# Performance work log

Hardware: AMD Instinct MI355X
Metric: run time of the kernel (lower is better)

The kernel has to match this reference:

```python
import jax, jax.numpy as jnp
import numpy as np

N, E = 50000, 800000
IN_FEATS, EDGE_FEATS = 256, 64
H, F = 8, 32  # num_heads, out_feats
LRELU_SLOPE = 0.01  # nn.LeakyReLU() default (module ignores alpha arg)


def setup_inputs() -> dict:
    key = jax.random.key(0)
    ks = jax.random.split(key, 9)
    return {
        "h": jax.random.normal(ks[0], (N, IN_FEATS), jnp.float32),
        "edge_features": jax.random.normal(ks[1], (E, EDGE_FEATS), jnp.float32),
        "src": jax.random.randint(ks[2], (E,), 0, N, jnp.int32),
        "dst": jax.random.randint(ks[3], (E,), 0, N, jnp.int32),
        "W_w": jax.random.normal(ks[4], (IN_FEATS, H * F), jnp.float32) * 0.05,
        "We_w": jax.random.normal(ks[5], (EDGE_FEATS, H * F), jnp.float32) * 0.05,
        "a_src": jax.random.normal(ks[6], (H, F), jnp.float32) * 0.1,
        "a_dst": jax.random.normal(ks[7], (H, F), jnp.float32) * 0.1,
        "a_edge": jax.random.normal(ks[8], (H, F), jnp.float32) * 0.1,
    }


def reference(h, edge_features, src, dst, W_w, We_w, a_src, a_dst, a_edge):
    # Node / edge linear projections -> [N,H,F], [E,H,F]
    Wh = (h @ W_w).reshape(-1, H, F)
    We = (edge_features @ We_w).reshape(-1, H, F)

    # Per-edge attention logits [E,H]: score = src.a_src + dst.a_dst + e.a_edge
    s = (jnp.einsum('ehf,hf->eh', Wh[src], a_src)
         + jnp.einsum('ehf,hf->eh', Wh[dst], a_dst)
         + jnp.einsum('ehf,hf->eh', We, a_edge))
    s = jnp.where(s > 0, s, LRELU_SLOPE * s)

    # Segment softmax over incoming edges of each dst node
    m = jax.ops.segment_max(s, dst, num_segments=N)          # [N,H]
    ex = jnp.exp(s - m[dst])                                 # [E,H]
    den = jax.ops.segment_sum(ex, dst, num_segments=N)       # [N,H]
    a = ex / den[dst]                                        # [E,H]

    # Weighted scatter-sum aggregation (dropout is identity at p=0 / eval)
    msg = Wh[src] * a[:, :, None]                            # [E,H,F]
    h_new = jax.ops.segment_sum(msg, dst, num_segments=N)    # [N,H,F]

    # concat=True path: reshape + ELU
    h_new = h_new.reshape(-1, H * F)
    return jax.nn.elu(h_new)
```

## Files before the change

### kernel.cpp

```cpp
#include <hip/hip_runtime.h>

#define N_NODES 50000
#define N_EDGES 800000
#define HEADS 8
#define FOUT 32
#define HF 256
#define IN_F 256
#define EDGE_F 64
#define SCAN_BLOCKS 196
#define HIST_BLOCKS 3125
#define CVTW_BLOCKS 256

typedef __attribute__((ext_vector_type(8))) short bf16x8;
typedef __attribute__((ext_vector_type(4))) float f32x4;

__device__ inline ushort f2bf(float f) {
  unsigned u = __float_as_uint(f);
  unsigned r = 0x7FFFu + ((u >> 16) & 1u);
  return (ushort)((u + r) >> 16);
}

__global__ __launch_bounds__(256) void k_misc(
    const int* __restrict__ dst, int* __restrict__ deg,
    const float* __restrict__ W, ushort* __restrict__ Wt,
    const float* __restrict__ We_w, const float* __restrict__ a_edge,
    float* __restrict__ Bmat)
{
  int b = blockIdx.x;
  if (b < HIST_BLOCKS) {
    int e = b * 256 + threadIdx.x;
    atomicAdd(&deg[dst[e]], 1);
  } else if (b < HIST_BLOCKS + CVTW_BLOCKS) {
    int i = (b - HIST_BLOCKS) * 256 + threadIdx.x;
    int n = i >> 8, k = i & 255;
    Wt[i] = f2bf(W[k * HF + n]);
  } else {
    int i = (b - HIST_BLOCKS - CVTW_BLOCKS) * 256 + threadIdx.x;
    if (i < EDGE_F * HEADS) {
      int k = i >> 3, h = i & 7;
      float s = 0.f;
#pragma unroll
      for (int f = 0; f < FOUT; ++f)
        s += We_w[k * HF + h * FOUT + f] * a_edge[h * FOUT + f];
      Bmat[i] = s;
    }
  }
}

__global__ __launch_bounds__(256) void k_gemm_fused(
    const float* __restrict__ A,
    const ushort* __restrict__ Wt,
    const float* __restrict__ a_src, const float* __restrict__ a_dst,
    ushort* __restrict__ Whb,
    float* __restrict__ alpha_s, float* __restrict__ alpha_d, int M)
{
  __shared__ ushort As[64 * 40];
  __shared__ ushort Bs[256 * 40];
  const int tid = threadIdx.x;
  const int wave = tid >> 6, lane = tid & 63;
  const int m0 = blockIdx.x * 64;
  const int row16 = lane & 15;
  const int kg = lane >> 4;
  f32x4 acc[4][4] = {};

  const int a_r = tid >> 2;
  const int a_c = (tid & 3) * 8;
  const int a_row = m0 + a_r;

  for (int k0 = 0; k0 < IN_F; k0 += 32) {
    uint4 av = make_uint4(0, 0, 0, 0);
    if (a_row < M) {
      float4 f0 = *(const float4*)&A[(size_t)a_row * IN_F + k0 + a_c];
      float4 f1 = *(const float4*)&A[(size_t)a_row * IN_F + k0 + a_c + 4];
      av.x = (unsigned)f2bf(f0.x) | ((unsigned)f2bf(f0.y) << 16);
      av.y = (unsigned)f2bf(f0.z) | ((unsigned)f2bf(f0.w) << 16);
      av.z = (unsigned)f2bf(f1.x) | ((unsigned)f2bf(f1.y) << 16);
      av.w = (unsigned)f2bf(f1.z) | ((unsigned)f2bf(f1.w) << 16);
    }
    *(uint4*)&As[a_r * 40 + a_c] = av;
    const uint4* bp = (const uint4*)&Wt[(size_t)tid * IN_F + k0];
    uint4 b0 = bp[0], b1 = bp[1];
    *(uint4*)&Bs[tid * 40 + 0] = b0;
    *(uint4*)&Bs[tid * 40 + 8] = b1;
    uint4 b2 = bp[2], b3 = bp[3];
    *(uint4*)&Bs[tid * 40 + 16] = b2;
    *(uint4*)&Bs[tid * 40 + 24] = b3;
    __syncthreads();
    bf16x8 af[4], bfr[4];
#pragma unroll
    for (int mi = 0; mi < 4; ++mi)
      af[mi] = *(const bf16x8*)&As[(mi * 16 + row16) * 40 + kg * 8];
#pragma unroll
    for (int ni = 0; ni < 4; ++ni)
      bfr[ni] = *(const bf16x8*)&Bs[(wave * 64 + ni * 16 + row16) * 40 + kg * 8];
#pragma unroll
    for (int mi = 0; mi < 4; ++mi)
#pragma unroll
      for (int ni = 0; ni < 4; ++ni)
        acc[mi][ni] = __builtin_amdgcn_mfma_f32_16x16x32_bf16(af[mi], bfr[ni], acc[mi][ni], 0, 0, 0);
    __syncthreads();
  }

  float cs[4], cd[4];
#pragma unroll
  for (int ni = 0; ni < 4; ++ni) {
    int hh = 2 * wave + (ni >> 1);
    int ff = (ni & 1) * 16 + row16;
    cs[ni] = a_src[hh * FOUT + ff];
    cd[ni] = a_dst[hh * FOUT + ff];
  }
#pragma unroll
  for (int mi = 0; mi < 4; ++mi) {
#pragma unroll
    for (int r = 0; r < 4; ++r) {
      int row = m0 + mi * 16 + kg * 4 + r;
      float ps0 = acc[mi][0][r] * cs[0] + acc[mi][1][r] * cs[1];
      float ps1 = acc[mi][2][r] * cs[2] + acc[mi][3][r] * cs[3];
      float pd0 = acc[mi][0][r] * cd[0] + acc[mi][1][r] * cd[1];
      float pd1 = acc[mi][2][r] * cd[2] + acc[mi][3][r] * cd[3];
#pragma unroll
      for (int msk = 1; msk <= 8; msk <<= 1) {
        ps0 += __shfl_xor(ps0, msk, 64);
        ps1 += __shfl_xor(ps1, msk, 64);
        pd0 += __shfl_xor(pd0, msk, 64);
        pd1 += __shfl_xor(pd1, msk, 64);
      }
      if (row16 == 0 && row < M) {
        *(float2*)&alpha_s[row * 8 + 2 * wave] = make_float2(ps0, ps1);
        *(float2*)&alpha_d[row * 8 + 2 * wave] = make_float2(pd0, pd1);
      }
      if (row < M) {
#pragma unroll
        for (int ni = 0; ni < 4; ++ni)
          Whb[(size_t)row * HF + wave * 64 + ni * 16 + row16] = f2bf(acc[mi][ni][r]);
      }
    }
  }
}

__global__ __launch_bounds__(256) void k_scanA(const int* __restrict__ deg,
                                               int* __restrict__ blockSums)
{
  __shared__ int ws[4];
  int idx = blockIdx.x * 256 + threadIdx.x;
  int v = (idx < N_NODES) ? deg[idx] : 0;
  int s = v;
#pragma unroll
  for (int off = 32; off > 0; off >>= 1)
    s += __shfl_xor(s, off, 64);
  if ((threadIdx.x & 63) == 0) ws[threadIdx.x >> 6] = s;
  __syncthreads();
  if (threadIdx.x == 0)
    blockSums[blockIdx.x] = ws[0] + ws[1] + ws[2] + ws[3];
}

__global__ __launch_bounds__(256) void k_scanC(const int* __restrict__ deg,
                                               const int* __restrict__ blockSums,
                                               int* __restrict__ offsets,
                                               int* __restrict__ cursor)
{
  __shared__ int tmp[256];
  __shared__ int s_base;
  int t = threadIdx.x;
  int v = (t < SCAN_BLOCKS) ? blockSums[t] : 0;
  tmp[t] = v;
  __syncthreads();
  int x = v;
  for (int off = 1; off < 256; off <<= 1) {
    int y = (t >= off) ? tmp[t - off] : 0;
    __syncthreads();
    x += y;
    tmp[t] = x;
    __syncthreads();
  }
  if (t == (int)blockIdx.x) s_base = x - v;
  if (blockIdx.x == 0 && t == 255) offsets[N_NODES] = x;
  __syncthreads();
  int base = s_base;
  int idx = blockIdx.x * 256 + t;
  int d = (idx < N_NODES) ? deg[idx] : 0;
  tmp[t] = d;
  __syncthreads();
  int x2 = d;
  for (int off = 1; off < 256; off <<= 1) {
    int y = (t >= off) ? tmp[t - off] : 0;
    __syncthreads();
    x2 += y;
    tmp[t] = x2;
    __syncthreads();
  }
  if (idx < N_NODES) {
    int pre = base + x2 - d;
    offsets[idx] = pre;
    cursor[idx] = pre;
  }
}

__global__ __launch_bounds__(256) void k_sedge(
    const float* __restrict__ ef, const int* __restrict__ src,
    const int* __restrict__ dst, const float* __restrict__ alpha_s,
    const float* __restrict__ alpha_d, const float* __restrict__ Bmat,
    int* __restrict__ cursor, float* __restrict__ s8,
    int2* __restrict__ srcE)
{
  __shared__ float Bs[EDGE_F * HEADS];
  for (int i = threadIdx.x; i < EDGE_F * HEADS; i += 256) Bs[i] = Bmat[i];
  __syncthreads();
  const int t = threadIdx.x;
  const int q = t & 3;
  const int e = blockIdx.x * 64 + (t >> 2);
  const int sn = src[e], dn = dst[e];

  float sc[8] = {};
  const float4* efr = (const float4*)&ef[(size_t)e * EDGE_F + q * 16];
#pragma unroll
  for (int g = 0; g < 4; ++g) {
    float4 v = efr[g];
    const float* b0 = &Bs[(q * 16 + g * 4) * 8];
#pragma unroll
    for (int hh = 0; hh < 8; ++hh)
      sc[hh] += v.x * b0[hh] + v.y * b0[8 + hh] + v.z * b0[16 + hh] + v.w * b0[24 + hh];
  }
#pragma unroll
  for (int hh = 0; hh < 8; ++hh) {
    sc[hh] += __shfl_xor(sc[hh], 1, 64);
    sc[hh] += __shfl_xor(sc[hh], 2, 64);
  }
  float2 as = *(const float2*)&alpha_s[sn * 8 + 2 * q];
  float2 ad = *(const float2*)&alpha_d[dn * 8 + 2 * q];
  float a0 = sc[2 * q] + as.x + ad.x;
  float a1 = sc[2 * q + 1] + as.y + ad.y;
  a0 = a0 > 0.f ? a0 : 0.01f * a0;
  a1 = a1 > 0.f ? a1 : 0.01f * a1;
  *(float2*)&s8[(size_t)e * 8 + 2 * q] = make_float2(a0, a1);
  if (q == 0) {
    int p = atomicAdd(&cursor[dn], 1);
    srcE[p] = make_int2(sn, e);
  }
}

__global__ __launch_bounds__(256) void k_agg(
    const float* __restrict__ s8, const int2* __restrict__ srcE,
    const int* __restrict__ offsets, const uint* __restrict__ Whb_u,
    float* __restrict__ out)
{
  const int n = blockIdx.x * 4 + (threadIdx.x >> 6);
  const int l = threadIdx.x & 63;
  const int beg = offsets[n], end = offsets[n + 1];
  const int h_sm = l & 7;
  const int es = l >> 3;
  const int h0 = l >> 4;
  const int h1 = 4 + h0;

  float m_run = -3.0e38f, l_run = 0.f;
  float acc00 = 0.f, acc01 = 0.f, acc10 = 0.f, acc11 = 0.f;

  int rx = 0;
  float s_cur = -3.0e38f;
  if (beg + es < end) {
    int2 r = srcE[beg + es];
    rx = r.x;
    s_cur = s8[(size_t)r.y * 8 + h_sm];
  }

  for (int c0 = beg; c0 < end; c0 += 8) {
    const int cnt = min(8, end - c0);
    int rx_n = 0;
    float s_n = -3.0e38f;
    if (c0 + 8 + es < end) {
      int2 r = srcE[c0 + 8 + es];
      rx_n = r.x;
      s_n = s8[(size_t)r.y * 8 + h_sm];
    }
    float s = s_cur;
    float mc = s;
    mc = fmaxf(mc, __shfl_xor(mc, 8, 64));
    mc = fmaxf(mc, __shfl_xor(mc, 16, 64));
    mc = fmaxf(mc, __shfl_xor(mc, 32, 64));
    float m_new = fmaxf(m_run, mc);
    float f = __expf(m_run - m_new);
    float w = __expf(s - m_new);
    float ws = w;
    ws += __shfl_xor(ws, 8, 64);
    ws += __shfl_xor(ws, 16, 64);
    ws += __shfl_xor(ws, 32, 64);
    l_run = l_run * f + ws;
    m_run = m_new;
    float f0 = __shfl(f, h0, 64);
    float f1 = __shfl(f, h1, 64);
    acc00 *= f0; acc01 *= f0; acc10 *= f1; acc11 *= f1;
    if (cnt == 8) {
#pragma unroll
      for (int k = 0; k < 8; ++k) {
        int idx = __shfl(rx, k << 3, 64);
        float w0 = __shfl(w, (k << 3) | h0, 64);
        float w1 = __shfl(w, (k << 3) | h1, 64);
        const uint* rowp = Whb_u + ((size_t)idx << 7);
        uint v0 = rowp[l];
        uint v1 = rowp[l + 64];
        acc00 = fmaf(w0, __uint_as_float(v0 << 16), acc00);
        acc01 = fmaf(w0, __uint_as_float(v0 & 0xFFFF0000u), acc01);
        acc10 = fmaf(w1, __uint_as_float(v1 << 16), acc10);
        acc11 = fmaf(w1, __uint_as_float(v1 & 0xFFFF0000u), acc11);
      }
    } else {
      for (int k = 0; k < cnt; ++k) {
        int idx = __shfl(rx, k << 3, 64);
        float w0 = __shfl(w, (k << 3) | h0, 64);
        float w1 = __shfl(w, (k << 3) | h1, 64);
        const uint* rowp = Whb_u + ((size_t)idx << 7);
        uint v0 = rowp[l];
        uint v1 = rowp[l + 64];
        acc00 = fmaf(w0, __uint_as_float(v0 << 16), acc00);
        acc01 = fmaf(w0, __uint_as_float(v0 & 0xFFFF0000u), acc01);
        acc10 = fmaf(w1, __uint_as_float(v1 << 16), acc10);
        acc11 = fmaf(w1, __uint_as_float(v1 & 0xFFFF0000u), acc11);
      }
    }
    rx = rx_n;
    s_cur = s_n;
  }

  float l0 = __shfl(l_run, h0, 64);
  float l1 = __shfl(l_run, h1, 64);
  float inv0 = (l0 > 0.f) ? 1.f / l0 : 0.f;
  float inv1 = (l1 > 0.f) ? 1.f / l1 : 0.f;
  acc00 *= inv0; acc01 *= inv0; acc10 *= inv1; acc11 *= inv1;

  float2 oA, oB;
  oA.x = acc00 > 0.f ? acc00 : expm1f(acc00);
  oA.y = acc01 > 0.f ? acc01 : expm1f(acc01);
  oB.x = acc10 > 0.f ? acc10 : expm1f(acc10);
  oB.y = acc11 > 0.f ? acc11 : expm1f(acc11);
  *(float2*)&out[(size_t)n * HF + 2 * l] = oA;
  *(float2*)&out[(size_t)n * HF + 128 + 2 * l] = oB;
}

extern "C" void kernel_launch(void* const* d_in, const int* in_sizes, int n_in,
                              void* d_out, int out_size, void* d_ws, size_t ws_size,
                              hipStream_t stream)
{
  const float* h    = (const float*)d_in[0];
  const float* ef   = (const float*)d_in[1];
  const int*   src  = (const int*)d_in[2];
  const int*   dst  = (const int*)d_in[3];
  const float* W_w  = (const float*)d_in[4];
  const float* We_w = (const float*)d_in[5];
  const float* a_s  = (const float*)d_in[6];
  const float* a_d  = (const float*)d_in[7];
  const float* a_e  = (const float*)d_in[8];
  float* out = (float*)d_out;

  char* ws = (char*)d_ws;
  size_t off = 0;
  auto take = [&](size_t bytes) {
    char* p = ws + off;
    off += (bytes + 255) & ~(size_t)255;
    return p;
  };
  ushort* Whb     = (ushort*)take((size_t)N_NODES * HF * 2);
  float* s8       = (float*)take((size_t)N_EDGES * HEADS * 4);
  float* alpha_s  = (float*)take((size_t)N_NODES * HEADS * 4);
  float* alpha_d  = (float*)take((size_t)N_NODES * HEADS * 4);
  int2*  srcE     = (int2*)take((size_t)N_EDGES * 8);
  int*   deg      = (int*)take((size_t)N_NODES * 4);
  int*   offs     = (int*)take((size_t)(N_NODES + 1) * 4);
  int*   cursor   = (int*)take((size_t)N_NODES * 4);
  float* Bmat     = (float*)take((size_t)EDGE_F * HEADS * 4);
  ushort* Wt      = (ushort*)take((size_t)HF * IN_F * 2);
  int*   blockSums= (int*)take((size_t)SCAN_BLOCKS * 4);

  (void)hipMemsetAsync(deg, 0, N_NODES * sizeof(int), stream);
  k_misc<<<HIST_BLOCKS + CVTW_BLOCKS + 2, 256, 0, stream>>>(dst, deg, W_w, Wt,
                                                            We_w, a_e, Bmat);
  k_scanA<<<SCAN_BLOCKS, 256, 0, stream>>>(deg, blockSums);
  k_scanC<<<SCAN_BLOCKS, 256, 0, stream>>>(deg, blockSums, offs, cursor);
  k_gemm_fused<<<(N_NODES + 63) / 64, 256, 0, stream>>>(h, Wt, a_s, a_d, Whb,
                                                        alpha_s, alpha_d, N_NODES);
  k_sedge<<<N_EDGES / 64, 256, 0, stream>>>(ef, src, dst, alpha_s, alpha_d,
                                            Bmat, cursor, s8, srcE);
  k_agg<<<N_NODES / 4, 256, 0, stream>>>(s8, srcE, offs, (const uint*)Whb, out);
}
```

Before: 247.9 us.

## Store edge scores in fp16 at CSR-sorted positions to coalesce aggregation reads

The edge scoring kernel now writes each edge's attention logits as fp16 directly into its dst-sorted CSR slot, so it stores only the source id instead of (src, edge id) pairs. The aggregation kernel then reads logits contiguously by CSR position rather than through an indirect gather by edge id, and moves half the bytes. This removes a random gather of scores and shrinks workspace traffic. The costs are scattered writes in the edge kernel and reduced logit precision, since fp16 rounding of pre-softmax scores can add error.

```diff
diff --git a/kernel.cpp b/kernel.cpp
--- a/kernel.cpp
+++ b/kernel.cpp
@@ -1,4 +1,5 @@
 #include <hip/hip_runtime.h>
+#include <hip/hip_fp16.h>
 
 #define N_NODES 50000
 #define N_EDGES 800000
@@ -200,8 +201,8 @@
     const float* __restrict__ ef, const int* __restrict__ src,
     const int* __restrict__ dst, const float* __restrict__ alpha_s,
     const float* __restrict__ alpha_d, const float* __restrict__ Bmat,
-    int* __restrict__ cursor, float* __restrict__ s8,
-    int2* __restrict__ srcE)
+    int* __restrict__ cursor, uint* __restrict__ s16u,
+    int* __restrict__ srcN)
 {
   __shared__ float Bs[EDGE_F * HEADS];
   for (int i = threadIdx.x; i < EDGE_F * HEADS; i += 256) Bs[i] = Bmat[i];
@@ -232,22 +233,23 @@
   float a1 = sc[2 * q + 1] + as.y + ad.y;
   a0 = a0 > 0.f ? a0 : 0.01f * a0;
   a1 = a1 > 0.f ? a1 : 0.01f * a1;
-  *(float2*)&s8[(size_t)e * 8 + 2 * q] = make_float2(a0, a1);
-  if (q == 0) {
-    int p = atomicAdd(&cursor[dn], 1);
-    srcE[p] = make_int2(sn, e);
-  }
+  uint hv = (uint)__half_as_ushort(__float2half_rn(a0)) |
+            ((uint)__half_as_ushort(__float2half_rn(a1)) << 16);
+  int p = 0;
+  if (q == 0) p = atomicAdd(&cursor[dn], 1);
+  p = __shfl(p, t & 60, 64);
+  s16u[(size_t)p * 4 + q] = hv;
+  if (q == 0) srcN[p] = sn;
 }
 
 __global__ __launch_bounds__(256) void k_agg(
-    const float* __restrict__ s8, const int2* __restrict__ srcE,
+    const ushort* __restrict__ s16, const int* __restrict__ srcN,
     const int* __restrict__ offsets, const uint* __restrict__ Whb_u,
     float* __restrict__ out)
 {
   const int n = blockIdx.x * 4 + (threadIdx.x >> 6);
   const int l = threadIdx.x & 63;
   const int beg = offsets[n], end = offsets[n + 1];
-  const int h_sm = l & 7;
   const int es = l >> 3;
   const int h0 = l >> 4;
   const int h1 = 4 + h0;
@@ -258,9 +260,8 @@
   int rx = 0;
   float s_cur = -3.0e38f;
   if (beg + es < end) {
-    int2 r = srcE[beg + es];
-    rx = r.x;
-    s_cur = s8[(size_t)r.y * 8 + h_sm];
+    rx = srcN[beg + es];
+    s_cur = __half2float(((const __half*)s16)[(size_t)beg * 8 + l]);
   }
 
   for (int c0 = beg; c0 < end; c0 += 8) {
@@ -268,9 +269,8 @@
     int rx_n = 0;
     float s_n = -3.0e38f;
     if (c0 + 8 + es < end) {
-      int2 r = srcE[c0 + 8 + es];
-      rx_n = r.x;
-      s_n = s8[(size_t)r.y * 8 + h_sm];
+      rx_n = srcN[c0 + 8 + es];
+      s_n = __half2float(((const __half*)s16)[(size_t)(c0 + 8) * 8 + l]);
     }
     float s = s_cur;
     float mc = s;
@@ -359,10 +359,10 @@
     return p;
   };
   ushort* Whb     = (ushort*)take((size_t)N_NODES * HF * 2);
-  float* s8       = (float*)take((size_t)N_EDGES * HEADS * 4);
+  uint*   s16u    = (uint*)take((size_t)N_EDGES * 8 * 2);
   float* alpha_s  = (float*)take((size_t)N_NODES * HEADS * 4);
   float* alpha_d  = (float*)take((size_t)N_NODES * HEADS * 4);
-  int2*  srcE     = (int2*)take((size_t)N_EDGES * 8);
+  int*   srcN     = (int*)take((size_t)N_EDGES * 4);
   int*   deg      = (int*)take((size_t)N_NODES * 4);
   int*   offs     = (int*)take((size_t)(N_NODES + 1) * 4);
   int*   cursor   = (int*)take((size_t)N_NODES * 4);
@@ -378,6 +378,7 @@
   k_gemm_fused<<<(N_NODES + 63) / 64, 256, 0, stream>>>(h, Wt, a_s, a_d, Whb,
                                                         alpha_s, alpha_d, N_NODES);
   k_sedge<<<N_EDGES / 64, 256, 0, stream>>>(ef, src, dst, alpha_s, alpha_d,
-                                            Bmat, cursor, s8, srcE);
-  k_agg<<<N_NODES / 4, 256, 0, stream>>>(s8, srcE, offs, (const uint*)Whb, out);
-}
+                                            Bmat, cursor, s16u, srcN);
+  k_agg<<<N_NODES / 4, 256, 0, stream>>>((const ushort*)s16u, srcN, offs,
+                                         (const uint*)Whb, out);
+}
```

New measurement: 242.8 us. -2.1%, faster.
